# Kernel tuning notes

Hardware: AMD Instinct MI355X
Metric: run time of the kernel (lower is better)

Reference implementation:

```python
import jax, jax.numpy as jnp
import numpy as np
import math

D_MODEL = 1024
N_HEADS = 16
HEAD_DIM = D_MODEL // N_HEADS
PAD_INDEX = 0
NEG_INF = -1e9  # matches torch masked_fill value


def setup_inputs() -> dict:
    key = jax.random.key(0)
    ks = jax.random.split(key, 10)
    b, s = 2, 2048
    x = jax.random.normal(ks[0], (b, s, D_MODEL), dtype=jnp.float32)
    input_ids = jax.random.randint(ks[1], (b, s), 0, 32000, dtype=jnp.int64)
    scale = 1.0 / math.sqrt(D_MODEL)
    def lin(k):
        kw, kb = jax.random.split(k)
        W = jax.random.uniform(kw, (D_MODEL, D_MODEL), jnp.float32, -scale, scale)
        bb = jax.random.uniform(kb, (D_MODEL,), jnp.float32, -scale, scale)
        return W, bb
    Wq, bq = lin(ks[2])
    Wk, bk = lin(ks[3])
    Wv, bv = lin(ks[4])
    Wo, bo = lin(ks[5])
    return {"x": x, "input_ids": input_ids,
            "Wq": Wq, "bq": bq, "Wk": Wk, "bk": bk,
            "Wv": Wv, "bv": bv, "Wo": Wo, "bo": bo}


def reference(x, input_ids, Wq, bq, Wk, bk, Wv, bv, Wo, bo):
    b, s, _ = x.shape
    # torch nn.Linear: y = x @ W.T + b
    q = (x @ Wq.T + bq).reshape(b, s, N_HEADS, HEAD_DIM)
    k = (x @ Wk.T + bk).reshape(b, s, N_HEADS, HEAD_DIM)
    v = (x @ Wv.T + bv).reshape(b, s, N_HEADS, HEAD_DIM)
    # scores: [b, h, s, s]
    scores = jnp.einsum('bqhd,bkhd->bhqk', q, k) / math.sqrt(HEAD_DIM)
    pad_mask = (input_ids != PAD_INDEX)[:, None, None, :]          # [b,1,1,s] over keys
    causal = jnp.tril(jnp.ones((s, s), dtype=bool))[None, None]     # [1,1,s,s]
    final_mask = pad_mask & causal
    scores = jnp.where(final_mask, scores, NEG_INF)
    attn = jax.nn.softmax(scores, axis=-1)
    out = jnp.einsum('bhqk,bkhd->bqhd', attn, v).reshape(b, s, D_MODEL)
    return out @ Wo.T + bo
```

## Files before the change

kernel.cpp:

```cpp
#include <hip/hip_runtime.h>

#define DMODEL 1024
#define NHEADS 16
#define HDIM   64
#define BATCH  2
#define SEQ    2048
#define MROWS  (BATCH*SEQ)

typedef __bf16 bf16x8 __attribute__((ext_vector_type(8)));
typedef __bf16 bf16x4 __attribute__((ext_vector_type(4)));
typedef float floatx4 __attribute__((ext_vector_type(4)));

typedef const __attribute__((address_space(1))) void gvoid;
typedef __attribute__((address_space(3))) void lvoid;

template<int V>  struct ICi { static constexpr int  value = V; };
template<bool V> struct ICb { static constexpr bool value = V; };

__global__ void cast_all(const float* __restrict__ x,
                         const float* __restrict__ wq, const float* __restrict__ wk,
                         const float* __restrict__ wv, const float* __restrict__ wo,
                         __bf16* __restrict__ xb, __bf16* __restrict__ wqb,
                         __bf16* __restrict__ wkb, __bf16* __restrict__ wvb,
                         __bf16* __restrict__ wob)
{
  const int i = blockIdx.x * 256 + threadIdx.x;
  const float* s; __bf16* o; int off;
  if (i < MROWS*DMODEL/4) { s = x; o = xb; off = i; }
  else {
    const int r = i - MROWS*DMODEL/4;
    const int w = r >> 18;
    off = r & 262143;
    s = (w == 0) ? wq : (w == 1) ? wk : (w == 2) ? wv : wo;
    o = (w == 0) ? wqb : (w == 1) ? wkb : (w == 2) ? wvb : wob;
  }
  const float4 f = ((const float4*)s)[off];
  bf16x4 v = {(__bf16)f.x, (__bf16)f.y, (__bf16)f.z, (__bf16)f.w};
  *(bf16x4*)(o + off*4) = v;
}

template<int MODE>
__global__ __launch_bounds__(256)
void gemm_nt(const unsigned short* __restrict__ A,
             const unsigned short* __restrict__ W0,
             const unsigned short* __restrict__ W1,
             const unsigned short* __restrict__ W2,
             const float* __restrict__ b0,
             const float* __restrict__ b1,
             const float* __restrict__ b2,
             unsigned short* __restrict__ qout,
             unsigned short* __restrict__ kout,
             unsigned short* __restrict__ vout,
             float* __restrict__ outf)
{
  const int K = DMODEL;
  __shared__ unsigned short As[128*32];
  __shared__ unsigned short Bs[128*32];
  const int tid  = threadIdx.x;
  const int wid  = tid >> 6;
  const int lane = tid & 63;

  const int lin = blockIdx.x;
  const int wg  = (MODE == 0) ? ((lin & 7)*96 + (lin >> 3))
                              : ((lin & 7)*32 + (lin >> 3));
  const int bx  = (MODE == 0) ? (wg % 24) : (wg & 7);
  const int by  = (MODE == 0) ? (wg / 24) : (wg >> 3);
  const int brow = by * 128;
  const int bcol = bx * 128;
  const int wr = (wid >> 1) * 64;
  const int wc = (wid & 1) * 64;

  int which = 0;
  const unsigned short* Bw = W0;
  const float* bias = b0;
  int bcolL = bcol;
  if (MODE == 0) {
    which = bcol >> 10;
    Bw   = which == 0 ? W0 : which == 1 ? W1 : W2;
    bias = which == 0 ? b0 : which == 1 ? b1 : b2;
    bcolL = bcol & 1023;
  }

  floatx4 acc[4][4] = {};

  const int sr = wid*16 + (lane >> 2);
  const int sc = (lane & 3) * 8;
  const int fr = lane & 15;
  const int fk = (lane >> 4) * 8;

  for (int kt = 0; kt < K; kt += 32) {
    __syncthreads();
#pragma unroll
    for (int i = 0; i < 2; ++i) {
      __builtin_amdgcn_global_load_lds(
          (gvoid*)(A + (size_t)(brow + i*64 + sr)*K + kt + sc),
          (lvoid*)(As + i*2048 + wid*512), 16, 0, 0);
      __builtin_amdgcn_global_load_lds(
          (gvoid*)(Bw + (size_t)(bcolL + i*64 + sr)*K + kt + sc),
          (lvoid*)(Bs + i*2048 + wid*512), 16, 0, 0);
    }
    __syncthreads();
    bf16x8 af[4], bfv[4];
#pragma unroll
    for (int m = 0; m < 4; ++m)
      af[m] = *(const bf16x8*)(As + (wr + m*16 + fr)*32 + fk);
#pragma unroll
    for (int n = 0; n < 4; ++n)
      bfv[n] = *(const bf16x8*)(Bs + (wc + n*16 + fr)*32 + fk);
#pragma unroll
    for (int m = 0; m < 4; ++m)
#pragma unroll
      for (int n = 0; n < 4; ++n)
        acc[m][n] = __builtin_amdgcn_mfma_f32_16x16x32_bf16(af[m], bfv[n], acc[m][n], 0, 0, 0);
  }

  const int er = (lane >> 4) * 4;
  const int ec = lane & 15;
#pragma unroll
  for (int m = 0; m < 4; ++m) {
#pragma unroll
    for (int n = 0; n < 4; ++n) {
      const int colL = bcolL + wc + n*16 + ec;
      const float bv = bias[colL];
      const int rowb = brow + wr + m*16 + er;
      if (MODE == 0) {
        const int bi = rowb >> 11, s = rowb & 2047;
        const int hh = colL >> 6, dd = colL & 63;
        if (which == 2) {
          bf16x4 v4 = {(__bf16)(acc[m][n][0] + bv), (__bf16)(acc[m][n][1] + bv),
                       (__bf16)(acc[m][n][2] + bv), (__bf16)(acc[m][n][3] + bv)};
          *(bf16x4*)((__bf16*)vout + ((size_t)(bi*NHEADS + hh)*HDIM + dd)*SEQ + s) = v4;
        } else {
          __bf16* o = (__bf16*)((which == 0) ? qout : kout);
#pragma unroll
          for (int j = 0; j < 4; ++j)
            o[((size_t)(bi*NHEADS + hh)*SEQ + s + j)*HDIM + dd] = (__bf16)(acc[m][n][j] + bv);
        }
      } else {
#pragma unroll
        for (int j = 0; j < 4; ++j)
          outf[(size_t)(rowb + j)*DMODEL + colL] = acc[m][n][j] + bv;
      }
    }
  }
}

__global__ __launch_bounds__(256, 2)
void attn_fwd(const unsigned short* __restrict__ qb,
              const unsigned short* __restrict__ kb,
              const unsigned short* __restrict__ vtb,
              const int* __restrict__ ids,
              unsigned short* __restrict__ outb)
{
  const int hb = blockIdx.x;
  const int pr = blockIdx.y;
  const int h = hb & 15, bi = hb >> 4;

  const int tid = threadIdx.x, wid = tid >> 6, lane = tid & 63;
  const size_t hoff = (size_t)(bi*NHEADS + h) * SEQ * HDIM;
  const unsigned short* Qh  = qb  + hoff;
  const unsigned short* Kh  = kb  + hoff;
  const unsigned short* Vth = vtb + hoff;

  __shared__ unsigned short Ks[2][128*64];
  __shared__ unsigned short Vs[2][64*128];
  __shared__ unsigned short Ps[4][16*128];

  const int q_   = lane & 15;
  const int hi4  = lane >> 4;
  const int koff = hi4 * 4;
  const float SC2 = 0.125f * 1.44269504088896f;

  const int krow0 = tid >> 3;
  const int ksw   = ((tid & 7) ^ ((tid >> 3) & 7)) * 8;
  const int vrow0 = tid >> 4;
  const int vsw   = ((tid & 15) ^ ((tid >> 4) & 7)) * 8;
  unsigned short* Pw = Ps[wid];

#define STAGE(T, B) do {                                                       \
    const unsigned short* kbase_ = Kh + (size_t)(T)*128*HDIM;                  \
    const unsigned short* vbase_ = Vth + (size_t)(T)*128;                      \
    _Pragma("unroll")                                                          \
    for (int i_ = 0; i_ < 4; ++i_)                                             \
      __builtin_amdgcn_global_load_lds(                                        \
          (gvoid*)(kbase_ + (size_t)(krow0 + i_*32)*HDIM + ksw),               \
          (lvoid*)(Ks[B] + (tid + i_*256)*8), 16, 0, 0);                       \
    _Pragma("unroll")                                                          \
    for (int i_ = 0; i_ < 4; ++i_)                                             \
      __builtin_amdgcn_global_load_lds(                                        \
          (gvoid*)(vbase_ + (size_t)(vrow0 + i_*16)*SEQ + vsw),                \
          (lvoid*)(Vs[B] + (tid + i_*256)*8), 16, 0, 0);                       \
  } while (0)

  for (int half = 0; half < 2; ++half) {
    const int qt = half ? 31 - pr : pr;
    const int qbase = qt * 64;
    const int qg = qbase + wid*16 + q_;
    bf16x8 qf[2];
#pragma unroll
    for (int c = 0; c < 2; ++c)
      qf[c] = *(const bf16x8*)(Qh + (size_t)qg*HDIM + c*32 + hi4*8);

    float lsum = 0.f;
    floatx4 Oacc[4] = {};

    auto step = [&](auto TLc, auto Mc, int kb0, int bufc,
                    unsigned long long wma, unsigned long long wmb) {
      constexpr int TL = decltype(TLc)::value;
      constexpr bool MASKED = decltype(Mc)::value;

      floatx4 st[TL];
      __builtin_amdgcn_s_setprio(1);
#pragma unroll
      for (int t = 0; t < TL; ++t) {
        st[t] = (floatx4){0.f, 0.f, 0.f, 0.f};
        const int kr = t*16 + q_;
#pragma unroll
        for (int c = 0; c < 2; ++c) {
          const int cd = ((c*4 + hi4) ^ (kr & 7)) * 8;
          bf16x8 kf = *(const bf16x8*)(Ks[bufc] + kr*64 + cd);
          st[t] = __builtin_amdgcn_mfma_f32_16x16x32_bf16(kf, qf[c], st[t], 0, 0, 0);
        }
      }
      __builtin_amdgcn_s_setprio(0);

      float ps = 0.f;
#pragma unroll
      for (int t = 0; t < TL; ++t) {
        float p[4];
#pragma unroll
        for (int r = 0; r < 4; ++r) {
          float pv = exp2f(st[t][r] * SC2);
          if (MASKED) {
            const int ko = t*16 + koff + r;
            const unsigned long long wm = (t < 4) ? wma : wmb;
            const bool dead = ((kb0 + ko) > qg) || (((wm >> (ko & 63)) & 1ull) != 0ull);
            pv = dead ? 0.f : pv;
          }
          p[r] = pv;
          ps += pv;
        }
        bf16x4 pk = {(__bf16)p[0], (__bf16)p[1], (__bf16)p[2], (__bf16)p[3]};
        const int cl = t*2 + (hi4 >> 1);
        *(bf16x4*)(Pw + q_*128 + ((cl ^ (q_ & 7)) * 8) + ((hi4 & 1) * 4)) = pk;
      }
      lsum += ps;

      __builtin_amdgcn_s_setprio(1);
#pragma unroll
      for (int ks = 0; ks < TL/2; ++ks) {
        const int cl = ks*4 + hi4;
        bf16x8 pf = *(const bf16x8*)(Pw + q_*128 + ((cl ^ (q_ & 7)) * 8));
#pragma unroll
        for (int n = 0; n < 4; ++n) {
          const int d = n*16 + q_;
          bf16x8 vf = *(const bf16x8*)(Vs[bufc] + d*128 + ((cl ^ (d & 7)) * 8));
          Oacc[n] = __builtin_amdgcn_mfma_f32_16x16x32_bf16(pf, vf, Oacc[n], 0, 0, 0);
        }
      }
      __builtin_amdgcn_s_setprio(0);
    };

    const int nT = (qt >> 1) + 1;
    STAGE(0, 0);

    for (int kbv = 0; kbv < nT; ++kbv) {
      const int kb0 = kbv * 128;
      const int bufc = kbv & 1;
      const bool last = (kbv == nT - 1);
      const int pv0 = ids[bi*SEQ + kb0 + lane];
      const int pv1 = ids[bi*SEQ + kb0 + 64 + lane];
      if (!last) {
        STAGE(kbv + 1, bufc ^ 1);
        asm volatile("s_waitcnt vmcnt(8)" ::: "memory");
      } else {
        asm volatile("s_waitcnt vmcnt(0)" ::: "memory");
      }
      const unsigned long long wma = __ballot(pv0 == 0);
      const unsigned long long wmb = __ballot(pv1 == 0);
      __builtin_amdgcn_s_barrier();
      __builtin_amdgcn_sched_barrier(0);

      if (!last) {
        if ((wma | wmb) == 0ull) step(ICi<8>{}, ICb<false>{}, kb0, bufc, 0ull, 0ull);
        else                     step(ICi<8>{}, ICb<true >{}, kb0, bufc, wma, wmb);
      } else {
        if (qt & 1) step(ICi<8>{}, ICb<true>{}, kb0, bufc, wma, wmb);
        else        step(ICi<4>{}, ICb<true>{}, kb0, bufc, wma, wmb);
      }
      __builtin_amdgcn_s_barrier();
    }

    float lt = lsum + __shfl_xor(lsum, 16);
    lt += __shfl_xor(lt, 32);

#pragma unroll
    for (int r = 0; r < 4; ++r) {
      const float inv = 1.f / __shfl(lt, koff + r);
      const int row = bi*SEQ + qbase + wid*16 + koff + r;
#pragma unroll
      for (int n = 0; n < 4; ++n)
        ((__bf16*)outb)[(size_t)row*DMODEL + h*HDIM + n*16 + q_] = (__bf16)(Oacc[n][r] * inv);
    }
  }
#undef STAGE
}

extern "C" void kernel_launch(void* const* d_in, const int* in_sizes, int n_in,
                              void* d_out, int out_size, void* d_ws, size_t ws_size,
                              hipStream_t stream)
{
  const float* x  = (const float*)d_in[0];
  const int*   ids= (const int*)d_in[1];
  const float* Wq = (const float*)d_in[2];
  const float* bq = (const float*)d_in[3];
  const float* Wk = (const float*)d_in[4];
  const float* bk = (const float*)d_in[5];
  const float* Wv = (const float*)d_in[6];
  const float* bv = (const float*)d_in[7];
  const float* Wo = (const float*)d_in[8];
  const float* bo = (const float*)d_in[9];
  float* out = (float*)d_out;

  char* ws = (char*)d_ws;
  unsigned short* xb   = (unsigned short*)(ws);
  unsigned short* wqb  = (unsigned short*)(ws + ( 8u<<20));
  unsigned short* wkb  = (unsigned short*)(ws + (10u<<20));
  unsigned short* wvb  = (unsigned short*)(ws + (12u<<20));
  unsigned short* wob  = (unsigned short*)(ws + (14u<<20));
  unsigned short* qbuf = (unsigned short*)(ws + (16u<<20));
  unsigned short* kbuf = (unsigned short*)(ws + (24u<<20));
  unsigned short* vbuf = (unsigned short*)(ws + (32u<<20));
  unsigned short* abuf = (unsigned short*)(ws + (40u<<20));

  cast_all<<<8192, 256, 0, stream>>>(x, Wq, Wk, Wv, Wo,
                                     (__bf16*)xb, (__bf16*)wqb, (__bf16*)wkb,
                                     (__bf16*)wvb, (__bf16*)wob);

  gemm_nt<0><<<768, 256, 0, stream>>>(xb, wqb, wkb, wvb, bq, bk, bv,
                                      qbuf, kbuf, vbuf, nullptr);

  attn_fwd<<<dim3(32, 16), 256, 0, stream>>>(qbuf, kbuf, vbuf, ids, abuf);

  gemm_nt<1><<<256, 256, 0, stream>>>(abuf, wob, wob, wob, bo, bo, bo,
                                      nullptr, nullptr, nullptr, out);
}
```

Baseline: 112.9 us.

## Double-buffer LDS tiles in projection GEMM to overlap global loads with MFMA

Converts the GEMM main loop to a two-stage pipeline. The next k-tile is loaded into a second LDS buffer through global_load_lds while MFMAs run on the current one, with explicit vmcnt waits and raw s_barriers in place of __syncthreads. It also raises wave priority around the MFMA block and adds an occupancy hint to launch bounds. The cost is doubled LDS use per block and reliance on manual waitcnt counting being correct.

```diff
diff --git a/kernel.cpp b/kernel.cpp
--- a/kernel.cpp
+++ b/kernel.cpp
@@ -40,7 +40,7 @@
 }
 
 template<int MODE>
-__global__ __launch_bounds__(256)
+__global__ __launch_bounds__(256, 3)
 void gemm_nt(const unsigned short* __restrict__ A,
              const unsigned short* __restrict__ W0,
              const unsigned short* __restrict__ W1,
@@ -54,8 +54,8 @@
              float* __restrict__ outf)
 {
   const int K = DMODEL;
-  __shared__ unsigned short As[128*32];
-  __shared__ unsigned short Bs[128*32];
+  __shared__ unsigned short As[2][128*32];
+  __shared__ unsigned short Bs[2][128*32];
   const int tid  = threadIdx.x;
   const int wid  = tid >> 6;
   const int lane = tid & 63;
@@ -88,31 +88,48 @@
   const int fr = lane & 15;
   const int fk = (lane >> 4) * 8;
 
+#define GSTAGE(KT, B) do {                                                     \
+    _Pragma("unroll")                                                          \
+    for (int i_ = 0; i_ < 2; ++i_) {                                           \
+      __builtin_amdgcn_global_load_lds(                                        \
+          (gvoid*)(A + (size_t)(brow + i_*64 + sr)*K + (KT) + sc),             \
+          (lvoid*)(As[B] + i_*2048 + wid*512), 16, 0, 0);                      \
+      __builtin_amdgcn_global_load_lds(                                        \
+          (gvoid*)(Bw + (size_t)(bcolL + i_*64 + sr)*K + (KT) + sc),           \
+          (lvoid*)(Bs[B] + i_*2048 + wid*512), 16, 0, 0);                      \
+    }                                                                          \
+  } while (0)
+
+  GSTAGE(0, 0);
+
   for (int kt = 0; kt < K; kt += 32) {
-    __syncthreads();
-#pragma unroll
-    for (int i = 0; i < 2; ++i) {
-      __builtin_amdgcn_global_load_lds(
-          (gvoid*)(A + (size_t)(brow + i*64 + sr)*K + kt + sc),
-          (lvoid*)(As + i*2048 + wid*512), 16, 0, 0);
-      __builtin_amdgcn_global_load_lds(
-          (gvoid*)(Bw + (size_t)(bcolL + i*64 + sr)*K + kt + sc),
-          (lvoid*)(Bs + i*2048 + wid*512), 16, 0, 0);
+    const int cur = (kt >> 5) & 1;
+    if (kt + 32 < K) {
+      GSTAGE(kt + 32, cur ^ 1);
+      asm volatile("s_waitcnt vmcnt(4)" ::: "memory");
+    } else {
+      asm volatile("s_waitcnt vmcnt(0)" ::: "memory");
     }
-    __syncthreads();
+    __builtin_amdgcn_s_barrier();
+    __builtin_amdgcn_sched_barrier(0);
+
     bf16x8 af[4], bfv[4];
 #pragma unroll
     for (int m = 0; m < 4; ++m)
-      af[m] = *(const bf16x8*)(As + (wr + m*16 + fr)*32 + fk);
+      af[m] = *(const bf16x8*)(As[cur] + (wr + m*16 + fr)*32 + fk);
 #pragma unroll
     for (int n = 0; n < 4; ++n)
-      bfv[n] = *(const bf16x8*)(Bs + (wc + n*16 + fr)*32 + fk);
+      bfv[n] = *(const bf16x8*)(Bs[cur] + (wc + n*16 + fr)*32 + fk);
+    __builtin_amdgcn_s_setprio(1);
 #pragma unroll
     for (int m = 0; m < 4; ++m)
 #pragma unroll
       for (int n = 0; n < 4; ++n)
         acc[m][n] = __builtin_amdgcn_mfma_f32_16x16x32_bf16(af[m], bfv[n], acc[m][n], 0, 0, 0);
-  }
+    __builtin_amdgcn_s_setprio(0);
+    __builtin_amdgcn_s_barrier();
+  }
+#undef GSTAGE
 
   const int er = (lane >> 4) * 4;
   const int ec = lane & 15;
```

Result: no change. 113.4 us (+0.4%).
